# Kernel tuning notes

Hardware: AMD Instinct MI355X
Metric: run time of the kernel (lower is better)

The kernel has to match this reference:

```python
import jax, jax.numpy as jnp
import numpy as np

N = 50000          # nodes
E = 1000000        # edges
EMB = 64           # emb_dim
L = 3              # num_layer
B = 250            # graphs (200 nodes each)
XF, EF = 7, 5      # node / edge feature dims
BN_EPS = 1e-5


def setup_inputs() -> dict:
    key = jax.random.key(0)
    ks = jax.random.split(key, 16)
    x = jax.random.normal(ks[0], (N, XF), dtype=jnp.float32)
    edge_attr = jax.random.normal(ks[1], (E, EF), dtype=jnp.float32)
    edge_index = jax.random.randint(ks[2], (2, E), 0, N, dtype=jnp.int32)
    # 250 contiguous graphs of 200 nodes: last node index of each graph
    last_idx = jnp.arange(1, B + 1, dtype=jnp.int32) * (N // B) - 1
    s = 0.05
    xW = jax.random.normal(ks[3], (XF, EMB), dtype=jnp.float32) * s
    xb = jnp.zeros((EMB,), dtype=jnp.float32)
    eW = jax.random.normal(ks[4], (L, EF, EMB), dtype=jnp.float32) * s
    eb = jnp.zeros((L, EMB), dtype=jnp.float32)
    W1 = jax.random.normal(ks[5], (L, EMB, 2 * EMB), dtype=jnp.float32) * s
    b1 = jnp.zeros((L, 2 * EMB), dtype=jnp.float32)
    W2 = jax.random.normal(ks[6], (L, 2 * EMB, EMB), dtype=jnp.float32) * s
    b2 = jnp.zeros((L, EMB), dtype=jnp.float32)
    gamma = jnp.ones((L, EMB), dtype=jnp.float32)
    beta = jnp.zeros((L, EMB), dtype=jnp.float32)
    return {"x": x, "edge_attr": edge_attr, "edge_index": edge_index,
            "last_idx": last_idx, "xW": xW, "xb": xb, "eW": eW, "eb": eb,
            "W1": W1, "b1": b1, "W2": W2, "b2": b2,
            "gamma": gamma, "beta": beta}


def _gnn_forward(x, edge_attr, edge_index, last_idx, xW, xb, eW, eb, W1, b1, W2, b2, gamma, beta):
    n = x.shape[0]
    # self-loop edge attrs: first column = 8, rest 0
    self_attr = jnp.zeros((n, EF), dtype=edge_attr.dtype).at[:, 0].set(8.0)
    ea = jnp.concatenate([edge_attr, self_attr], axis=0)          # [E+N, EF]
    loop = jnp.arange(n, dtype=edge_index.dtype)
    src = jnp.concatenate([edge_index[0], loop])                  # x_j indices
    dst = jnp.concatenate([edge_index[1], loop])                  # aggregation targets

    h = x @ xW + xb                                               # [N, EMB]
    for l in range(L):
        e = ea @ eW[l] + eb[l]                                    # [E+N, EMB]
        msg = h[src] + e                                          # gather + combine
        agg = jax.ops.segment_sum(msg, dst, num_segments=n)       # scatter-add
        h2 = jax.nn.relu(agg @ W1[l] + b1[l]) @ W2[l] + b2[l]     # GIN MLP
        mean = jnp.mean(h2, axis=0)
        var = jnp.mean(jnp.square(h2 - mean), axis=0)             # biased, like torch BN
        hn = (h2 - mean) * jax.lax.rsqrt(var + BN_EPS) * gamma[l] + beta[l]
        h = jax.nn.elu(hn) if l < L - 1 else hn                   # drop_ratio = 0
    return h[last_idx]                                            # super-node reps [B, EMB]


def reference(x, edge_attr, edge_index, last_idx, xW, xb, eW, eb, W1, b1, W2, b2, gamma, beta):
    return _gnn_forward(x, edge_attr, edge_index, last_idx, xW, xb, eW, eb, W1, b1, W2, b2, gamma, beta)
```

## Files before the change

### kernel.cpp

```cpp
#include <hip/hip_runtime.h>

#define N_NODES 50000
#define N_EDGES 1000000
#define EMB     64
#define HID     128
#define NLAYER  3
#define NGRAPH  250
#define XFD     7
#define EFD     5
#define BN_EPS  1e-5f

#define BKT_SH 8
#define BKT_SZ 256
#define NBKT   ((N_NODES + BKT_SZ - 1) / BKT_SZ)
#define CHKE   4096
#define NCHK   ((N_EDGES + CHKE - 1) / CHKE)
#define CNTM   (NBKT * NCHK)
#define NB2    ((CNTM + 255) / 256)

__device__ __forceinline__ void atomAddF(float* p, float v) {
    __hip_atomic_fetch_add(p, v, __ATOMIC_RELAXED, __HIP_MEMORY_SCOPE_AGENT);
}

__device__ __forceinline__ unsigned short f2bf(float f) {
    unsigned int u = __float_as_uint(f);
    u += 0x7fffu + ((u >> 16) & 1u);
    return (unsigned short)(u >> 16);
}
__device__ __forceinline__ float bf2f(unsigned short s) {
    return __uint_as_float(((unsigned int)s) << 16);
}
__device__ __forceinline__ float4 bf4(ushort4 u) {
    return make_float4(bf2f(u.x), bf2f(u.y), bf2f(u.z), bf2f(u.w));
}

__global__ void k_input(const float* __restrict__ x, const float* __restrict__ xW,
                        const float* __restrict__ xb, unsigned short* __restrict__ h) {
    int gid = blockIdx.x * 256 + threadIdx.x;
    if (gid >= N_NODES * EMB) return;
    int n = gid >> 6, f = gid & 63;
    float acc = xb[f];
#pragma unroll
    for (int k = 0; k < XFD; ++k) acc = fmaf(x[n * XFD + k], xW[k * EMB + f], acc);
    h[gid] = f2bf(acc);
}

__global__ __launch_bounds__(256) void k_binA(const int* __restrict__ dst,
                                              int* __restrict__ cntmat) {
    __shared__ int hist[NBKT];
    int tid = threadIdx.x, c = blockIdx.x;
    for (int i = tid; i < NBKT; i += 256) hist[i] = 0;
    __syncthreads();
    int e0 = c * CHKE, e1 = min(e0 + CHKE, N_EDGES);
    for (int i = e0 + tid; i < e1; i += 256) atomicAdd(&hist[dst[i] >> BKT_SH], 1);
    __syncthreads();
    for (int b = tid; b < NBKT; b += 256) cntmat[b * NCHK + c] = hist[b];
}

__global__ __launch_bounds__(256) void k_gscanA(const int* __restrict__ in, int n,
                                                int* __restrict__ bsum) {
    int tid = threadIdx.x, lane = tid & 63, wid = tid >> 6;
    int i = blockIdx.x * 256 + tid;
    int v = (i < n) ? in[i] : 0;
#pragma unroll
    for (int off = 32; off; off >>= 1) v += __shfl_down(v, off);
    __shared__ int ws[4];
    if (lane == 0) ws[wid] = v;
    __syncthreads();
    if (tid == 0) bsum[blockIdx.x] = ws[0] + ws[1] + ws[2] + ws[3];
}

__global__ __launch_bounds__(256) void k_gscanB(const int* __restrict__ bsum, int nb,
                                                int* __restrict__ boff) {
    int tid = threadIdx.x, lane = tid & 63, wid = tid >> 6;
    int v = (tid < nb) ? bsum[tid] : 0;
    int x = v;
#pragma unroll
    for (int off = 1; off < 64; off <<= 1) {
        int y = __shfl_up(x, off);
        if (lane >= off) x += y;
    }
    __shared__ int wtot[4];
    if (lane == 63) wtot[wid] = x;
    __syncthreads();
    int woff = 0;
    for (int w = 0; w < wid; ++w) woff += wtot[w];
    if (tid < nb) boff[tid] = woff + x - v;
}

__global__ __launch_bounds__(256) void k_gscanC(const int* __restrict__ in, int n,
                                                const int* __restrict__ boff,
                                                int* __restrict__ out) {
    int tid = threadIdx.x, lane = tid & 63, wid = tid >> 6;
    int i = blockIdx.x * 256 + tid;
    int v = (i < n) ? in[i] : 0;
    int x = v;
#pragma unroll
    for (int off = 1; off < 64; off <<= 1) {
        int y = __shfl_up(x, off);
        if (lane >= off) x += y;
    }
    __shared__ int wtot[4];
    if (lane == 63) wtot[wid] = x;
    __syncthreads();
    int woff = boff[blockIdx.x];
    for (int w = 0; w < wid; ++w) woff += wtot[w];
    if (i < n) out[i] = woff + x - v;
}

__global__ __launch_bounds__(256) void k_binC(const int* __restrict__ src,
                                              const int* __restrict__ dst,
                                              const int* __restrict__ off2,
                                              int2* __restrict__ bufSD) {
    __shared__ int cur[NBKT];
    int tid = threadIdx.x, c = blockIdx.x;
    for (int b = tid; b < NBKT; b += 256) cur[b] = off2[b * NCHK + c];
    __syncthreads();
    int e0 = c * CHKE, e1 = min(e0 + CHKE, N_EDGES);
    for (int i = e0 + tid; i < e1; i += 256) {
        int d = dst[i];
        int b = d >> BKT_SH;
        int p = atomicAdd(&cur[b], 1);
        bufSD[p] = make_int2(src[i], ((d & (BKT_SZ - 1)) << 20) | i);
    }
}

__global__ __launch_bounds__(256) void k_binD(const int2* __restrict__ bufSD,
                                              const int* __restrict__ off2,
                                              int* __restrict__ csr,
                                              int* __restrict__ csrE,
                                              int* __restrict__ rowstart) {
    __shared__ int hist[BKT_SZ];
    __shared__ int cur[BKT_SZ];
    __shared__ int wtot[4];
    int tid = threadIdx.x, b = blockIdx.x;
    int bstart = off2[b * NCHK];
    int bend = (b + 1 < NBKT) ? off2[(b + 1) * NCHK] : N_EDGES;
    hist[tid] = 0;
    __syncthreads();
    for (int j = bstart + tid; j < bend; j += 256)
        atomicAdd(&hist[bufSD[j].y >> 20], 1);
    __syncthreads();
    int lane = tid & 63, wid = tid >> 6;
    int v = hist[tid], x = v;
#pragma unroll
    for (int off = 1; off < 64; off <<= 1) {
        int y = __shfl_up(x, off);
        if (lane >= off) x += y;
    }
    if (lane == 63) wtot[wid] = x;
    __syncthreads();
    int woff = 0;
    for (int w = 0; w < wid; ++w) woff += wtot[w];
    int ex = woff + x - v;
    cur[tid] = ex;
    int node = b * BKT_SZ + tid;
    if (node < N_NODES) rowstart[node] = bstart + ex;
    if (b == NBKT - 1 && tid == 0) rowstart[N_NODES] = N_EDGES;
    __syncthreads();
    for (int j = bstart + tid; j < bend; j += 256) {
        int2 t = bufSD[j];
        int local = t.y >> 20;
        int p = atomicAdd(&cur[local], 1);
        csr[bstart + p] = t.x;
        csrE[bstart + p] = t.y & 0xFFFFF;
    }
}

__global__ __launch_bounds__(256) void k_aggE(const int* __restrict__ rowstart,
                                              const int* __restrict__ csrE,
                                              const float* __restrict__ ea,
                                              float* __restrict__ aggE) {
    int wid = (blockIdx.x * 256 + threadIdx.x) >> 6;
    int lane = threadIdx.x & 63;
    if (wid >= N_NODES) return;
    int j0 = rowstart[wid], j1 = rowstart[wid + 1];
    float s0 = 0.f, s1 = 0.f, s2 = 0.f, s3 = 0.f, s4 = 0.f;
    for (int j = j0 + lane; j < j1; j += 64) {
        int e = csrE[j];
        const float* p = ea + (size_t)e * EFD;
        s0 += p[0]; s1 += p[1]; s2 += p[2]; s3 += p[3]; s4 += p[4];
    }
#pragma unroll
    for (int off = 32; off; off >>= 1) {
        s0 += __shfl_down(s0, off);
        s1 += __shfl_down(s1, off);
        s2 += __shfl_down(s2, off);
        s3 += __shfl_down(s3, off);
        s4 += __shfl_down(s4, off);
    }
    if (lane == 0) {
        float* o = aggE + (size_t)wid * EFD;
        o[0] = s0; o[1] = s1; o[2] = s2; o[3] = s3; o[4] = s4;
    }
}

__global__ __launch_bounds__(256) void k_agg(const unsigned short* __restrict__ h,
                                             float* __restrict__ agg,
                                             const int* __restrict__ rowstart,
                                             const int* __restrict__ csr,
                                             const float* __restrict__ aggE,
                                             const float* __restrict__ eWl,
                                             const float* __restrict__ ebl) {
    int wid = (blockIdx.x * 256 + threadIdx.x) >> 6;
    int lane = threadIdx.x & 63;
    if (wid >= N_NODES) return;
    int n = wid;
    int lg = lane >> 4, lq = lane & 15;
    const ushort4* hb = (const ushort4*)h;
    int j0 = rowstart[n], j1 = rowstart[n + 1];
    float4 acc = make_float4(0.f, 0.f, 0.f, 0.f);
    int j = j0;
    while (j < j1) {
        int take = j1 - j;
        if (take > 64) take = 64;
        int myid = (lane < take) ? csr[j + lane] : 0;
        int nt = (take + 3) >> 2;
        int t = 0;
        for (; t + 4 <= nt; t += 4) {
            int e0 = t * 4 + lg, e1 = e0 + 4, e2 = e0 + 8, e3 = e0 + 12;
            int s0 = __shfl(myid, e0), s1 = __shfl(myid, e1),
                s2 = __shfl(myid, e2), s3 = __shfl(myid, e3);
            ushort4 u0 = hb[(size_t)s0 * 16 + lq];
            ushort4 u1 = hb[(size_t)s1 * 16 + lq];
            ushort4 u2 = hb[(size_t)s2 * 16 + lq];
            ushort4 u3 = hb[(size_t)s3 * 16 + lq];
            float4 v0 = bf4(u0), v1 = bf4(u1), v2 = bf4(u2), v3 = bf4(u3);
            if (e0 < take) { acc.x += v0.x; acc.y += v0.y; acc.z += v0.z; acc.w += v0.w; }
            if (e1 < take) { acc.x += v1.x; acc.y += v1.y; acc.z += v1.z; acc.w += v1.w; }
            if (e2 < take) { acc.x += v2.x; acc.y += v2.y; acc.z += v2.z; acc.w += v2.w; }
            if (e3 < take) { acc.x += v3.x; acc.y += v3.y; acc.z += v3.z; acc.w += v3.w; }
        }
        for (; t < nt; ++t) {
            int e = t * 4 + lg;
            int s = __shfl(myid, e);
            float4 v = bf4(hb[(size_t)s * 16 + lq]);
            if (e < take) { acc.x += v.x; acc.y += v.y; acc.z += v.z; acc.w += v.w; }
        }
        j += take;
    }
    acc.x += __shfl_xor(acc.x, 16); acc.y += __shfl_xor(acc.y, 16);
    acc.z += __shfl_xor(acc.z, 16); acc.w += __shfl_xor(acc.w, 16);
    acc.x += __shfl_xor(acc.x, 32); acc.y += __shfl_xor(acc.y, 32);
    acc.z += __shfl_xor(acc.z, 32); acc.w += __shfl_xor(acc.w, 32);
    const float4* eW4 = (const float4*)eWl;
    float4 ew0 = eW4[lq], ew1 = eW4[16 + lq], ew2 = eW4[32 + lq],
           ew3 = eW4[48 + lq], ew4 = eW4[64 + lq];
    float4 eb4 = ((const float4*)ebl)[lq];
    float a0 = aggE[n * 5 + 0], a1 = aggE[n * 5 + 1], a2 = aggE[n * 5 + 2],
          a3 = aggE[n * 5 + 3], a4 = aggE[n * 5 + 4];
    float c0 = a0 + 8.f;
    float ce = (float)(j1 - j0) + 1.f;
    float4 bb = bf4(hb[(size_t)n * 16 + lq]);
    bb.x = fmaf(c0, ew0.x, bb.x); bb.y = fmaf(c0, ew0.y, bb.y);
    bb.z = fmaf(c0, ew0.z, bb.z); bb.w = fmaf(c0, ew0.w, bb.w);
    bb.x = fmaf(a1, ew1.x, bb.x); bb.y = fmaf(a1, ew1.y, bb.y);
    bb.z = fmaf(a1, ew1.z, bb.z); bb.w = fmaf(a1, ew1.w, bb.w);
    bb.x = fmaf(a2, ew2.x, bb.x); bb.y = fmaf(a2, ew2.y, bb.y);
    bb.z = fmaf(a2, ew2.z, bb.z); bb.w = fmaf(a2, ew2.w, bb.w);
    bb.x = fmaf(a3, ew3.x, bb.x); bb.y = fmaf(a3, ew3.y, bb.y);
    bb.z = fmaf(a3, ew3.z, bb.z); bb.w = fmaf(a3, ew3.w, bb.w);
    bb.x = fmaf(a4, ew4.x, bb.x); bb.y = fmaf(a4, ew4.y, bb.y);
    bb.z = fmaf(a4, ew4.z, bb.z); bb.w = fmaf(a4, ew4.w, bb.w);
    bb.x = fmaf(ce, eb4.x, bb.x); bb.y = fmaf(ce, eb4.y, bb.y);
    bb.z = fmaf(ce, eb4.z, bb.z); bb.w = fmaf(ce, eb4.w, bb.w);
    if (lg == 0) {
        ((float4*)agg)[(size_t)n * 16 + lq] =
            make_float4(acc.x + bb.x, acc.y + bb.y, acc.z + bb.z, acc.w + bb.w);
    }
}

__global__ __launch_bounds__(256) void k_mlp1(const float* __restrict__ agg,
                                              unsigned short* __restrict__ hidden,
                                              const float* __restrict__ W1l,
                                              const float* __restrict__ b1l) {
    __shared__ float w1s[64 * 128];
    __shared__ float as[32 * 68];
    __shared__ float b1s[128];
    int tid = threadIdx.x;
    int n0 = blockIdx.x * 32;
    const float4* wg = (const float4*)W1l;
    float4* wsh = (float4*)w1s;
#pragma unroll
    for (int i = 0; i < 8; ++i) wsh[tid + i * 256] = wg[tid + i * 256];
    if (tid < 128) b1s[tid] = b1l[tid];
    const float4* ag4 = (const float4*)agg;
#pragma unroll
    for (int i = 0; i < 2; ++i) {
        int idx = tid + i * 256;
        int m = idx >> 4, kq = idx & 15;
        int nn = n0 + m;
        float4 v = make_float4(0.f, 0.f, 0.f, 0.f);
        if (nn < N_NODES) v = ag4[nn * 16 + kq];
        *(float4*)&as[m * 68 + kq * 4] = v;
    }
    __syncthreads();
    int j0 = (tid & 31) * 4;
    int m0 = (tid >> 5) * 4;
    float acc[4][4] = {};
#pragma unroll 8
    for (int k = 0; k < 64; ++k) {
        float4 w = *(const float4*)&w1s[k * 128 + j0];
        float a0 = as[(m0 + 0) * 68 + k];
        float a1 = as[(m0 + 1) * 68 + k];
        float a2 = as[(m0 + 2) * 68 + k];
        float a3 = as[(m0 + 3) * 68 + k];
        acc[0][0] = fmaf(a0, w.x, acc[0][0]); acc[0][1] = fmaf(a0, w.y, acc[0][1]);
        acc[0][2] = fmaf(a0, w.z, acc[0][2]); acc[0][3] = fmaf(a0, w.w, acc[0][3]);
        acc[1][0] = fmaf(a1, w.x, acc[1][0]); acc[1][1] = fmaf(a1, w.y, acc[1][1]);
        acc[1][2] = fmaf(a1, w.z, acc[1][2]); acc[1][3] = fmaf(a1, w.w, acc[1][3]);
        acc[2][0] = fmaf(a2, w.x, acc[2][0]); acc[2][1] = fmaf(a2, w.y, acc[2][1]);
        acc[2][2] = fmaf(a2, w.z, acc[2][2]); acc[2][3] = fmaf(a2, w.w, acc[2][3]);
        acc[3][0] = fmaf(a3, w.x, acc[3][0]); acc[3][1] = fmaf(a3, w.y, acc[3][1]);
        acc[3][2] = fmaf(a3, w.z, acc[3][2]); acc[3][3] = fmaf(a3, w.w, acc[3][3]);
    }
    ushort4* hid4 = (ushort4*)hidden;
#pragma unroll
    for (int a = 0; a < 4; ++a) {
        int nn = n0 + m0 + a;
        if (nn < N_NODES) {
            ushort4 o;
            o.x = f2bf(fmaxf(acc[a][0] + b1s[j0 + 0], 0.f));
            o.y = f2bf(fmaxf(acc[a][1] + b1s[j0 + 1], 0.f));
            o.z = f2bf(fmaxf(acc[a][2] + b1s[j0 + 2], 0.f));
            o.w = f2bf(fmaxf(acc[a][3] + b1s[j0 + 3], 0.f));
            hid4[(size_t)nn * 32 + (j0 >> 2)] = o;
        }
    }
}

__global__ __launch_bounds__(256) void k_mlp2(const unsigned short* __restrict__ hidden,
                                              float* __restrict__ h2,
                                              const float* __restrict__ W2l,
                                              const float* __restrict__ b2l,
                                              float* __restrict__ stats) {
    __shared__ float w2s[128 * 64];
    __shared__ float hs[64 * 132];
    __shared__ float b2s[64];
    int tid = threadIdx.x;
    int n0 = blockIdx.x * 64;
    const float4* wg = (const float4*)W2l;
    float4* wsh = (float4*)w2s;
#pragma unroll
    for (int i = 0; i < 8; ++i) wsh[tid + i * 256] = wg[tid + i * 256];
    if (tid < 64) b2s[tid] = b2l[tid];
    const ushort4* hb4 = (const ushort4*)hidden;
#pragma unroll
    for (int i = 0; i < 8; ++i) {
        int idx = tid + i * 256;
        int m = idx >> 5, kq = idx & 31;
        int nn = n0 + m;
        float4 v = make_float4(0.f, 0.f, 0.f, 0.f);
        if (nn < N_NODES) v = bf4(hb4[(size_t)nn * 32 + kq]);
        *(float4*)&hs[m * 132 + kq * 4] = v;
    }
    __syncthreads();
    int f0 = (tid & 15) * 4;
    int m0 = (tid >> 4) * 4;
    float acc[4][4] = {};
#pragma unroll 8
    for (int k = 0; k < 128; ++k) {
        float4 w = *(const float4*)&w2s[k * 64 + f0];
        float a0 = hs[(m0 + 0) * 132 + k];
        float a1 = hs[(m0 + 1) * 132 + k];
        float a2 = hs[(m0 + 2) * 132 + k];
        float a3 = hs[(m0 + 3) * 132 + k];
        acc[0][0] = fmaf(a0, w.x, acc[0][0]); acc[0][1] = fmaf(a0, w.y, acc[0][1]);
        acc[0][2] = fmaf(a0, w.z, acc[0][2]); acc[0][3] = fmaf(a0, w.w, acc[0][3]);
        acc[1][0] = fmaf(a1, w.x, acc[1][0]); acc[1][1] = fmaf(a1, w.y, acc[1][1]);
        acc[1][2] = fmaf(a1, w.z, acc[1][2]); acc[1][3] = fmaf(a1, w.w, acc[1][3]);
        acc[2][0] = fmaf(a2, w.x, acc[2][0]); acc[2][1] = fmaf(a2, w.y, acc[2][1]);
        acc[2][2] = fmaf(a2, w.z, acc[2][2]); acc[2][3] = fmaf(a2, w.w, acc[2][3]);
        acc[3][0] = fmaf(a3, w.x, acc[3][0]); acc[3][1] = fmaf(a3, w.y, acc[3][1]);
        acc[3][2] = fmaf(a3, w.z, acc[3][2]); acc[3][3] = fmaf(a3, w.w, acc[3][3]);
    }
    float sf[4] = {0.f, 0.f, 0.f, 0.f}, qf[4] = {0.f, 0.f, 0.f, 0.f};
#pragma unroll
    for (int a = 0; a < 4; ++a) {
        int nn = n0 + m0 + a;
        if (nn < N_NODES) {
            float v0 = acc[a][0] + b2s[f0 + 0];
            float v1 = acc[a][1] + b2s[f0 + 1];
            float v2 = acc[a][2] + b2s[f0 + 2];
            float v3 = acc[a][3] + b2s[f0 + 3];
            *(float4*)&h2[nn * EMB + f0] = make_float4(v0, v1, v2, v3);
            sf[0] += v0; sf[1] += v1; sf[2] += v2; sf[3] += v3;
            qf[0] = fmaf(v0, v0, qf[0]); qf[1] = fmaf(v1, v1, qf[1]);
            qf[2] = fmaf(v2, v2, qf[2]); qf[3] = fmaf(v3, v3, qf[3]);
        }
    }
    __syncthreads();
    float* red = hs;
    int mg = tid >> 4;
#pragma unroll
    for (int j = 0; j < 4; ++j) {
        red[mg * 64 + f0 + j] = sf[j];
        red[1024 + mg * 64 + f0 + j] = qf[j];
    }
    __syncthreads();
    if (tid < 64) {
        float s = 0.f, q = 0.f;
#pragma unroll
        for (int m = 0; m < 16; ++m) {
            s += red[m * 64 + tid];
            q += red[1024 + m * 64 + tid];
        }
        atomAddF(&stats[tid], s);
        atomAddF(&stats[64 + tid], q);
    }
}

__global__ void k_bn(const float* __restrict__ h2, unsigned short* __restrict__ h,
                     const float* __restrict__ stats, const float* __restrict__ gam,
                     const float* __restrict__ bet) {
    int gid = blockIdx.x * 256 + threadIdx.x;
    if (gid >= N_NODES * EMB) return;
    int f = gid & 63;
    const float invN = 1.f / (float)N_NODES;
    float mean = stats[f] * invN;
    float var = stats[64 + f] * invN - mean * mean;
    float inv = rsqrtf(var + BN_EPS);
    float v = (h2[gid] - mean) * inv * gam[f] + bet[f];
    h[gid] = f2bf(v > 0.f ? v : expm1f(v));
}

__global__ void k_bnout(const float* __restrict__ h2, const int* __restrict__ last,
                        const float* __restrict__ stats, const float* __restrict__ gam,
                        const float* __restrict__ bet, float* __restrict__ out) {
    int gid = blockIdx.x * 256 + threadIdx.x;
    if (gid >= NGRAPH * EMB) return;
    int b = gid >> 6, f = gid & 63;
    const float invN = 1.f / (float)N_NODES;
    float mean = stats[f] * invN;
    float var = stats[64 + f] * invN - mean * mean;
    float inv = rsqrtf(var + BN_EPS);
    out[gid] = (h2[last[b] * EMB + f] - mean) * inv * gam[f] + bet[f];
}

extern "C" void kernel_launch(void* const* d_in, const int* in_sizes, int n_in,
                              void* d_out, int out_size, void* d_ws, size_t ws_size,
                              hipStream_t stream) {
    const float* x   = (const float*)d_in[0];
    const float* ea  = (const float*)d_in[1];
    const int*   eidx= (const int*)d_in[2];
    const int*   last= (const int*)d_in[3];
    const float* xW  = (const float*)d_in[4];
    const float* xb  = (const float*)d_in[5];
    const float* eW  = (const float*)d_in[6];
    const float* eb  = (const float*)d_in[7];
    const float* W1  = (const float*)d_in[8];
    const float* b1  = (const float*)d_in[9];
    const float* W2  = (const float*)d_in[10];
    const float* b2  = (const float*)d_in[11];
    const float* gam = (const float*)d_in[12];
    const float* bet = (const float*)d_in[13];
    float* out = (float*)d_out;

    const int* srcI = eidx;
    const int* dstI = eidx + N_EDGES;

    float* hslot  = (float*)d_ws;
    float* agg    = hslot + N_NODES * EMB;
    float* hidslot= agg + N_NODES * EMB;
    float* aggE   = hidslot + N_NODES * HID;
    float* stats  = aggE + NBKT * BKT_SZ * EFD;
    int* rowstart = (int*)(stats + NLAYER * 2 * EMB);
    int* csr      = rowstart + N_NODES + 1;
    int* cntmat   = csr + N_EDGES;
    int* off2     = cntmat + CNTM;
    int* bsum     = off2 + CNTM;
    int* boff     = bsum + NB2;
    unsigned short* h      = (unsigned short*)hslot;
    unsigned short* hidden = (unsigned short*)hidslot;
    int2* bufSD   = (int2*)agg;
    int*  csrE    = (int*)hidslot;

    hipMemsetAsync(stats, 0, NLAYER * 2 * EMB * sizeof(float), stream);

    k_input<<<(N_NODES * EMB + 255) / 256, 256, 0, stream>>>(x, xW, xb, h);
    k_binA<<<NCHK, 256, 0, stream>>>(dstI, cntmat);
    k_gscanA<<<NB2, 256, 0, stream>>>(cntmat, CNTM, bsum);
    k_gscanB<<<1, 256, 0, stream>>>(bsum, NB2, boff);
    k_gscanC<<<NB2, 256, 0, stream>>>(cntmat, CNTM, boff, off2);
    k_binC<<<NCHK, 256, 0, stream>>>(srcI, dstI, off2, bufSD);
    k_binD<<<NBKT, 256, 0, stream>>>(bufSD, off2, csr, csrE, rowstart);
    k_aggE<<<(N_NODES * 64 + 255) / 256, 256, 0, stream>>>(rowstart, csrE, ea, aggE);

    for (int l = 0; l < NLAYER; ++l) {
        k_agg<<<(N_NODES * 64 + 255) / 256, 256, 0, stream>>>(
            h, agg, rowstart, csr, aggE, eW + l * EFD * EMB, eb + l * EMB);
        k_mlp1<<<(N_NODES + 31) / 32, 256, 0, stream>>>(agg, hidden, W1 + l * EMB * HID,
                                                        b1 + l * HID);
        k_mlp2<<<(N_NODES + 63) / 64, 256, 0, stream>>>(hidden, agg, W2 + l * HID * EMB,
                                                        b2 + l * EMB, stats + l * 2 * EMB);
        if (l < NLAYER - 1) {
            k_bn<<<(N_NODES * EMB + 255) / 256, 256, 0, stream>>>(
                agg, h, stats + l * 2 * EMB, gam + l * EMB, bet + l * EMB);
        } else {
            k_bnout<<<(NGRAPH * EMB + 255) / 256, 256, 0, stream>>>(
                agg, last, stats + l * 2 * EMB, gam + l * EMB, bet + l * EMB, out);
        }
    }
}
```

Baseline: 409.3 us.

## Fuse GIN MLP layers into one kernel with bf16 LDS staging; batch agg nodes

Merges the two MLP kernels into a single k_mlp. The 128-wide hidden activation now stays in shared memory instead of making a round trip through global memory. Weights, inputs and the hidden tile are staged as bf16 in LDS, with transposed activation layouts, to keep shared-memory use down. k_agg now handles four nodes per wave so the edge-weight and bias loads are amortised, which reduces wave count and parallelism in the gather. The costs are lower precision for the MLP inputs and weights, higher LDS use per block, and k_mlp reading and writing the same agg buffer under __restrict__.

```diff
diff --git a/kernel.cpp b/kernel.cpp
--- a/kernel.cpp
+++ b/kernel.cpp
@@ -202,195 +202,186 @@
                                              const float* __restrict__ aggE,
                                              const float* __restrict__ eWl,
                                              const float* __restrict__ ebl) {
-    int wid = (blockIdx.x * 256 + threadIdx.x) >> 6;
+    int wave = (blockIdx.x * 256 + threadIdx.x) >> 6;
     int lane = threadIdx.x & 63;
-    if (wid >= N_NODES) return;
-    int n = wid;
+    int nbase = wave * 4;
+    if (nbase >= N_NODES) return;
     int lg = lane >> 4, lq = lane & 15;
     const ushort4* hb = (const ushort4*)h;
-    int j0 = rowstart[n], j1 = rowstart[n + 1];
-    float4 acc = make_float4(0.f, 0.f, 0.f, 0.f);
-    int j = j0;
-    while (j < j1) {
-        int take = j1 - j;
-        if (take > 64) take = 64;
-        int myid = (lane < take) ? csr[j + lane] : 0;
-        int nt = (take + 3) >> 2;
-        int t = 0;
-        for (; t + 4 <= nt; t += 4) {
-            int e0 = t * 4 + lg, e1 = e0 + 4, e2 = e0 + 8, e3 = e0 + 12;
-            int s0 = __shfl(myid, e0), s1 = __shfl(myid, e1),
-                s2 = __shfl(myid, e2), s3 = __shfl(myid, e3);
-            ushort4 u0 = hb[(size_t)s0 * 16 + lq];
-            ushort4 u1 = hb[(size_t)s1 * 16 + lq];
-            ushort4 u2 = hb[(size_t)s2 * 16 + lq];
-            ushort4 u3 = hb[(size_t)s3 * 16 + lq];
-            float4 v0 = bf4(u0), v1 = bf4(u1), v2 = bf4(u2), v3 = bf4(u3);
-            if (e0 < take) { acc.x += v0.x; acc.y += v0.y; acc.z += v0.z; acc.w += v0.w; }
-            if (e1 < take) { acc.x += v1.x; acc.y += v1.y; acc.z += v1.z; acc.w += v1.w; }
-            if (e2 < take) { acc.x += v2.x; acc.y += v2.y; acc.z += v2.z; acc.w += v2.w; }
-            if (e3 < take) { acc.x += v3.x; acc.y += v3.y; acc.z += v3.z; acc.w += v3.w; }
-        }
-        for (; t < nt; ++t) {
-            int e = t * 4 + lg;
-            int s = __shfl(myid, e);
-            float4 v = bf4(hb[(size_t)s * 16 + lq]);
-            if (e < take) { acc.x += v.x; acc.y += v.y; acc.z += v.z; acc.w += v.w; }
-        }
-        j += take;
-    }
-    acc.x += __shfl_xor(acc.x, 16); acc.y += __shfl_xor(acc.y, 16);
-    acc.z += __shfl_xor(acc.z, 16); acc.w += __shfl_xor(acc.w, 16);
-    acc.x += __shfl_xor(acc.x, 32); acc.y += __shfl_xor(acc.y, 32);
-    acc.z += __shfl_xor(acc.z, 32); acc.w += __shfl_xor(acc.w, 32);
     const float4* eW4 = (const float4*)eWl;
     float4 ew0 = eW4[lq], ew1 = eW4[16 + lq], ew2 = eW4[32 + lq],
            ew3 = eW4[48 + lq], ew4 = eW4[64 + lq];
     float4 eb4 = ((const float4*)ebl)[lq];
-    float a0 = aggE[n * 5 + 0], a1 = aggE[n * 5 + 1], a2 = aggE[n * 5 + 2],
-          a3 = aggE[n * 5 + 3], a4 = aggE[n * 5 + 4];
-    float c0 = a0 + 8.f;
-    float ce = (float)(j1 - j0) + 1.f;
-    float4 bb = bf4(hb[(size_t)n * 16 + lq]);
-    bb.x = fmaf(c0, ew0.x, bb.x); bb.y = fmaf(c0, ew0.y, bb.y);
-    bb.z = fmaf(c0, ew0.z, bb.z); bb.w = fmaf(c0, ew0.w, bb.w);
-    bb.x = fmaf(a1, ew1.x, bb.x); bb.y = fmaf(a1, ew1.y, bb.y);
-    bb.z = fmaf(a1, ew1.z, bb.z); bb.w = fmaf(a1, ew1.w, bb.w);
-    bb.x = fmaf(a2, ew2.x, bb.x); bb.y = fmaf(a2, ew2.y, bb.y);
-    bb.z = fmaf(a2, ew2.z, bb.z); bb.w = fmaf(a2, ew2.w, bb.w);
-    bb.x = fmaf(a3, ew3.x, bb.x); bb.y = fmaf(a3, ew3.y, bb.y);
-    bb.z = fmaf(a3, ew3.z, bb.z); bb.w = fmaf(a3, ew3.w, bb.w);
-    bb.x = fmaf(a4, ew4.x, bb.x); bb.y = fmaf(a4, ew4.y, bb.y);
-    bb.z = fmaf(a4, ew4.z, bb.z); bb.w = fmaf(a4, ew4.w, bb.w);
-    bb.x = fmaf(ce, eb4.x, bb.x); bb.y = fmaf(ce, eb4.y, bb.y);
-    bb.z = fmaf(ce, eb4.z, bb.z); bb.w = fmaf(ce, eb4.w, bb.w);
-    if (lg == 0) {
-        ((float4*)agg)[(size_t)n * 16 + lq] =
-            make_float4(acc.x + bb.x, acc.y + bb.y, acc.z + bb.z, acc.w + bb.w);
-    }
-}
-
-__global__ __launch_bounds__(256) void k_mlp1(const float* __restrict__ agg,
-                                              unsigned short* __restrict__ hidden,
-                                              const float* __restrict__ W1l,
-                                              const float* __restrict__ b1l) {
-    __shared__ float w1s[64 * 128];
-    __shared__ float as[32 * 68];
+    int nend = min(nbase + 4, N_NODES);
+    for (int n = nbase; n < nend; ++n) {
+        int j0 = rowstart[n], j1 = rowstart[n + 1];
+        float4 acc = make_float4(0.f, 0.f, 0.f, 0.f);
+        int j = j0;
+        while (j < j1) {
+            int take = j1 - j;
+            if (take > 64) take = 64;
+            int myid = (lane < take) ? csr[j + lane] : 0;
+            int nt = (take + 3) >> 2;
+            int t = 0;
+            for (; t + 4 <= nt; t += 4) {
+                int e0 = t * 4 + lg, e1 = e0 + 4, e2 = e0 + 8, e3 = e0 + 12;
+                int s0 = __shfl(myid, e0), s1 = __shfl(myid, e1),
+                    s2 = __shfl(myid, e2), s3 = __shfl(myid, e3);
+                float4 v0 = bf4(hb[(size_t)s0 * 16 + lq]);
+                float4 v1 = bf4(hb[(size_t)s1 * 16 + lq]);
+                float4 v2 = bf4(hb[(size_t)s2 * 16 + lq]);
+                float4 v3 = bf4(hb[(size_t)s3 * 16 + lq]);
+                if (e0 < take) { acc.x += v0.x; acc.y += v0.y; acc.z += v0.z; acc.w += v0.w; }
+                if (e1 < take) { acc.x += v1.x; acc.y += v1.y; acc.z += v1.z; acc.w += v1.w; }
+                if (e2 < take) { acc.x += v2.x; acc.y += v2.y; acc.z += v2.z; acc.w += v2.w; }
+                if (e3 < take) { acc.x += v3.x; acc.y += v3.y; acc.z += v3.z; acc.w += v3.w; }
+            }
+            for (; t < nt; ++t) {
+                int e = t * 4 + lg;
+                int s = __shfl(myid, e);
+                float4 v = bf4(hb[(size_t)s * 16 + lq]);
+                if (e < take) { acc.x += v.x; acc.y += v.y; acc.z += v.z; acc.w += v.w; }
+            }
+            j += take;
+        }
+        acc.x += __shfl_xor(acc.x, 16); acc.y += __shfl_xor(acc.y, 16);
+        acc.z += __shfl_xor(acc.z, 16); acc.w += __shfl_xor(acc.w, 16);
+        acc.x += __shfl_xor(acc.x, 32); acc.y += __shfl_xor(acc.y, 32);
+        acc.z += __shfl_xor(acc.z, 32); acc.w += __shfl_xor(acc.w, 32);
+        float a0 = aggE[n * 5 + 0], a1 = aggE[n * 5 + 1], a2 = aggE[n * 5 + 2],
+              a3 = aggE[n * 5 + 3], a4 = aggE[n * 5 + 4];
+        float c0 = a0 + 8.f;
+        float ce = (float)(j1 - j0) + 1.f;
+        float4 bb = bf4(hb[(size_t)n * 16 + lq]);
+        bb.x = fmaf(c0, ew0.x, bb.x); bb.y = fmaf(c0, ew0.y, bb.y);
+        bb.z = fmaf(c0, ew0.z, bb.z); bb.w = fmaf(c0, ew0.w, bb.w);
+        bb.x = fmaf(a1, ew1.x, bb.x); bb.y = fmaf(a1, ew1.y, bb.y);
+        bb.z = fmaf(a1, ew1.z, bb.z); bb.w = fmaf(a1, ew1.w, bb.w);
+        bb.x = fmaf(a2, ew2.x, bb.x); bb.y = fmaf(a2, ew2.y, bb.y);
+        bb.z = fmaf(a2, ew2.z, bb.z); bb.w = fmaf(a2, ew2.w, bb.w);
+        bb.x = fmaf(a3, ew3.x, bb.x); bb.y = fmaf(a3, ew3.y, bb.y);
+        bb.z = fmaf(a3, ew3.z, bb.z); bb.w = fmaf(a3, ew3.w, bb.w);
+        bb.x = fmaf(a4, ew4.x, bb.x); bb.y = fmaf(a4, ew4.y, bb.y);
+        bb.z = fmaf(a4, ew4.z, bb.z); bb.w = fmaf(a4, ew4.w, bb.w);
+        bb.x = fmaf(ce, eb4.x, bb.x); bb.y = fmaf(ce, eb4.y, bb.y);
+        bb.z = fmaf(ce, eb4.z, bb.z); bb.w = fmaf(ce, eb4.w, bb.w);
+        if (lg == 0) {
+            ((float4*)agg)[(size_t)n * 16 + lq] =
+                make_float4(acc.x + bb.x, acc.y + bb.y, acc.z + bb.z, acc.w + bb.w);
+        }
+    }
+}
+
+__global__ __launch_bounds__(256) void k_mlp(const float* __restrict__ agg,
+                                             float* __restrict__ h2,
+                                             const float* __restrict__ W1l,
+                                             const float* __restrict__ b1l,
+                                             const float* __restrict__ W2l,
+                                             const float* __restrict__ b2l,
+                                             float* __restrict__ stats) {
+    __shared__ unsigned short w1s[64 * 128];
+    __shared__ unsigned short w2s[128 * 64];
+    __shared__ unsigned short asT[64 * 68];
+    __shared__ unsigned short hidT[128 * 68];
     __shared__ float b1s[128];
+    __shared__ float b2s[64];
     int tid = threadIdx.x;
-    int n0 = blockIdx.x * 32;
-    const float4* wg = (const float4*)W1l;
-    float4* wsh = (float4*)w1s;
-#pragma unroll
-    for (int i = 0; i < 8; ++i) wsh[tid + i * 256] = wg[tid + i * 256];
+    int n0 = blockIdx.x * 64;
+    const float4* wg1 = (const float4*)W1l;
+    const float4* wg2 = (const float4*)W2l;
+    ushort4* w1v = (ushort4*)w1s;
+    ushort4* w2v = (ushort4*)w2s;
+#pragma unroll
+    for (int i = 0; i < 8; ++i) {
+        float4 v1 = wg1[tid + i * 256];
+        w1v[tid + i * 256] = make_ushort4(f2bf(v1.x), f2bf(v1.y), f2bf(v1.z), f2bf(v1.w));
+        float4 v2 = wg2[tid + i * 256];
+        w2v[tid + i * 256] = make_ushort4(f2bf(v2.x), f2bf(v2.y), f2bf(v2.z), f2bf(v2.w));
+    }
     if (tid < 128) b1s[tid] = b1l[tid];
+    if (tid < 64) b2s[tid] = b2l[tid];
     const float4* ag4 = (const float4*)agg;
 #pragma unroll
-    for (int i = 0; i < 2; ++i) {
+    for (int i = 0; i < 4; ++i) {
         int idx = tid + i * 256;
         int m = idx >> 4, kq = idx & 15;
         int nn = n0 + m;
         float4 v = make_float4(0.f, 0.f, 0.f, 0.f);
-        if (nn < N_NODES) v = ag4[nn * 16 + kq];
-        *(float4*)&as[m * 68 + kq * 4] = v;
-    }
-    __syncthreads();
-    int j0 = (tid & 31) * 4;
-    int m0 = (tid >> 5) * 4;
-    float acc[4][4] = {};
-#pragma unroll 8
-    for (int k = 0; k < 64; ++k) {
-        float4 w = *(const float4*)&w1s[k * 128 + j0];
-        float a0 = as[(m0 + 0) * 68 + k];
-        float a1 = as[(m0 + 1) * 68 + k];
-        float a2 = as[(m0 + 2) * 68 + k];
-        float a3 = as[(m0 + 3) * 68 + k];
-        acc[0][0] = fmaf(a0, w.x, acc[0][0]); acc[0][1] = fmaf(a0, w.y, acc[0][1]);
-        acc[0][2] = fmaf(a0, w.z, acc[0][2]); acc[0][3] = fmaf(a0, w.w, acc[0][3]);
-        acc[1][0] = fmaf(a1, w.x, acc[1][0]); acc[1][1] = fmaf(a1, w.y, acc[1][1]);
-        acc[1][2] = fmaf(a1, w.z, acc[1][2]); acc[1][3] = fmaf(a1, w.w, acc[1][3]);
-        acc[2][0] = fmaf(a2, w.x, acc[2][0]); acc[2][1] = fmaf(a2, w.y, acc[2][1]);
-        acc[2][2] = fmaf(a2, w.z, acc[2][2]); acc[2][3] = fmaf(a2, w.w, acc[2][3]);
-        acc[3][0] = fmaf(a3, w.x, acc[3][0]); acc[3][1] = fmaf(a3, w.y, acc[3][1]);
-        acc[3][2] = fmaf(a3, w.z, acc[3][2]); acc[3][3] = fmaf(a3, w.w, acc[3][3]);
-    }
-    ushort4* hid4 = (ushort4*)hidden;
-#pragma unroll
-    for (int a = 0; a < 4; ++a) {
-        int nn = n0 + m0 + a;
+        if (nn < N_NODES) v = ag4[(size_t)nn * 16 + kq];
+        asT[(kq * 4 + 0) * 68 + m] = f2bf(v.x);
+        asT[(kq * 4 + 1) * 68 + m] = f2bf(v.y);
+        asT[(kq * 4 + 2) * 68 + m] = f2bf(v.z);
+        asT[(kq * 4 + 3) * 68 + m] = f2bf(v.w);
+    }
+    __syncthreads();
+    {
+        int j0 = (tid & 31) * 4;
+        int m0 = (tid >> 5) * 8;
+        float acc1[8][4] = {};
+#pragma unroll 4
+        for (int k = 0; k < 64; ++k) {
+            float4 w = bf4(((const ushort4*)w1s)[k * 32 + (j0 >> 2)]);
+            float4 av0 = bf4(*(const ushort4*)&asT[k * 68 + m0]);
+            float4 av1 = bf4(*(const ushort4*)&asT[k * 68 + m0 + 4]);
+            float a[8] = {av0.x, av0.y, av0.z, av0.w, av1.x, av1.y, av1.z, av1.w};
+#pragma unroll
+            for (int i = 0; i < 8; ++i) {
+                acc1[i][0] = fmaf(a[i], w.x, acc1[i][0]);
+                acc1[i][1] = fmaf(a[i], w.y, acc1[i][1]);
+                acc1[i][2] = fmaf(a[i], w.z, acc1[i][2]);
+                acc1[i][3] = fmaf(a[i], w.w, acc1[i][3]);
+            }
+        }
+#pragma unroll
+        for (int c = 0; c < 4; ++c) {
+            float bv = b1s[j0 + c];
+            ushort4 o1, o2;
+            o1.x = f2bf(fmaxf(acc1[0][c] + bv, 0.f));
+            o1.y = f2bf(fmaxf(acc1[1][c] + bv, 0.f));
+            o1.z = f2bf(fmaxf(acc1[2][c] + bv, 0.f));
+            o1.w = f2bf(fmaxf(acc1[3][c] + bv, 0.f));
+            o2.x = f2bf(fmaxf(acc1[4][c] + bv, 0.f));
+            o2.y = f2bf(fmaxf(acc1[5][c] + bv, 0.f));
+            o2.z = f2bf(fmaxf(acc1[6][c] + bv, 0.f));
+            o2.w = f2bf(fmaxf(acc1[7][c] + bv, 0.f));
+            *(ushort4*)&hidT[(j0 + c) * 68 + m0] = o1;
+            *(ushort4*)&hidT[(j0 + c) * 68 + m0 + 4] = o2;
+        }
+    }
+    __syncthreads();
+    int f0 = (tid & 15) * 4;
+    int m0p = (tid >> 4) * 4;
+    float acc2[4][4] = {};
+#pragma unroll 4
+    for (int k = 0; k < 128; ++k) {
+        float4 w = bf4(((const ushort4*)w2s)[k * 16 + (f0 >> 2)]);
+        float4 a = bf4(*(const ushort4*)&hidT[k * 68 + m0p]);
+        acc2[0][0] = fmaf(a.x, w.x, acc2[0][0]); acc2[0][1] = fmaf(a.x, w.y, acc2[0][1]);
+        acc2[0][2] = fmaf(a.x, w.z, acc2[0][2]); acc2[0][3] = fmaf(a.x, w.w, acc2[0][3]);
+        acc2[1][0] = fmaf(a.y, w.x, acc2[1][0]); acc2[1][1] = fmaf(a.y, w.y, acc2[1][1]);
+        acc2[1][2] = fmaf(a.y, w.z, acc2[1][2]); acc2[1][3] = fmaf(a.y, w.w, acc2[1][3]);
+        acc2[2][0] = fmaf(a.z, w.x, acc2[2][0]); acc2[2][1] = fmaf(a.z, w.y, acc2[2][1]);
+        acc2[2][2] = fmaf(a.z, w.z, acc2[2][2]); acc2[2][3] = fmaf(a.z, w.w, acc2[2][3]);
+        acc2[3][0] = fmaf(a.w, w.x, acc2[3][0]); acc2[3][1] = fmaf(a.w, w.y, acc2[3][1]);
+        acc2[3][2] = fmaf(a.w, w.z, acc2[3][2]); acc2[3][3] = fmaf(a.w, w.w, acc2[3][3]);
+    }
+    float sf[4] = {0.f, 0.f, 0.f, 0.f}, qf[4] = {0.f, 0.f, 0.f, 0.f};
+#pragma unroll
+    for (int i = 0; i < 4; ++i) {
+        int nn = n0 + m0p + i;
         if (nn < N_NODES) {
-            ushort4 o;
-            o.x = f2bf(fmaxf(acc[a][0] + b1s[j0 + 0], 0.f));
-            o.y = f2bf(fmaxf(acc[a][1] + b1s[j0 + 1], 0.f));
-            o.z = f2bf(fmaxf(acc[a][2] + b1s[j0 + 2], 0.f));
-            o.w = f2bf(fmaxf(acc[a][3] + b1s[j0 + 3], 0.f));
-            hid4[(size_t)nn * 32 + (j0 >> 2)] = o;
-        }
-    }
-}
-
-__global__ __launch_bounds__(256) void k_mlp2(const unsigned short* __restrict__ hidden,
-                                              float* __restrict__ h2,
-                                              const float* __restrict__ W2l,
-                                              const float* __restrict__ b2l,
-                                              float* __restrict__ stats) {
-    __shared__ float w2s[128 * 64];
-    __shared__ float hs[64 * 132];
-    __shared__ float b2s[64];
-    int tid = threadIdx.x;
-    int n0 = blockIdx.x * 64;
-    const float4* wg = (const float4*)W2l;
-    float4* wsh = (float4*)w2s;
-#pragma unroll
-    for (int i = 0; i < 8; ++i) wsh[tid + i * 256] = wg[tid + i * 256];
-    if (tid < 64) b2s[tid] = b2l[tid];
-    const ushort4* hb4 = (const ushort4*)hidden;
-#pragma unroll
-    for (int i = 0; i < 8; ++i) {
-        int idx = tid + i * 256;
-        int m = idx >> 5, kq = idx & 31;
-        int nn = n0 + m;
-        float4 v = make_float4(0.f, 0.f, 0.f, 0.f);
-        if (nn < N_NODES) v = bf4(hb4[(size_t)nn * 32 + kq]);
-        *(float4*)&hs[m * 132 + kq * 4] = v;
-    }
-    __syncthreads();
-    int f0 = (tid & 15) * 4;
-    int m0 = (tid >> 4) * 4;
-    float acc[4][4] = {};
-#pragma unroll 8
-    for (int k = 0; k < 128; ++k) {
-        float4 w = *(const float4*)&w2s[k * 64 + f0];
-        float a0 = hs[(m0 + 0) * 132 + k];
-        float a1 = hs[(m0 + 1) * 132 + k];
-        float a2 = hs[(m0 + 2) * 132 + k];
-        float a3 = hs[(m0 + 3) * 132 + k];
-        acc[0][0] = fmaf(a0, w.x, acc[0][0]); acc[0][1] = fmaf(a0, w.y, acc[0][1]);
-        acc[0][2] = fmaf(a0, w.z, acc[0][2]); acc[0][3] = fmaf(a0, w.w, acc[0][3]);
-        acc[1][0] = fmaf(a1, w.x, acc[1][0]); acc[1][1] = fmaf(a1, w.y, acc[1][1]);
-        acc[1][2] = fmaf(a1, w.z, acc[1][2]); acc[1][3] = fmaf(a1, w.w, acc[1][3]);
-        acc[2][0] = fmaf(a2, w.x, acc[2][0]); acc[2][1] = fmaf(a2, w.y, acc[2][1]);
-        acc[2][2] = fmaf(a2, w.z, acc[2][2]); acc[2][3] = fmaf(a2, w.w, acc[2][3]);
-        acc[3][0] = fmaf(a3, w.x, acc[3][0]); acc[3][1] = fmaf(a3, w.y, acc[3][1]);
-        acc[3][2] = fmaf(a3, w.z, acc[3][2]); acc[3][3] = fmaf(a3, w.w, acc[3][3]);
-    }
-    float sf[4] = {0.f, 0.f, 0.f, 0.f}, qf[4] = {0.f, 0.f, 0.f, 0.f};
-#pragma unroll
-    for (int a = 0; a < 4; ++a) {
-        int nn = n0 + m0 + a;
-        if (nn < N_NODES) {
-            float v0 = acc[a][0] + b2s[f0 + 0];
-            float v1 = acc[a][1] + b2s[f0 + 1];
-            float v2 = acc[a][2] + b2s[f0 + 2];
-            float v3 = acc[a][3] + b2s[f0 + 3];
-            *(float4*)&h2[nn * EMB + f0] = make_float4(v0, v1, v2, v3);
+            float v0 = acc2[i][0] + b2s[f0 + 0];
+            float v1 = acc2[i][1] + b2s[f0 + 1];
+            float v2 = acc2[i][2] + b2s[f0 + 2];
+            float v3 = acc2[i][3] + b2s[f0 + 3];
+            *(float4*)&h2[(size_t)nn * EMB + f0] = make_float4(v0, v1, v2, v3);
             sf[0] += v0; sf[1] += v1; sf[2] += v2; sf[3] += v3;
             qf[0] = fmaf(v0, v0, qf[0]); qf[1] = fmaf(v1, v1, qf[1]);
             qf[2] = fmaf(v2, v2, qf[2]); qf[3] = fmaf(v3, v3, qf[3]);
         }
     }
     __syncthreads();
-    float* red = hs;
+    float* red = (float*)hidT;
     int mg = tid >> 4;
 #pragma unroll
     for (int j = 0; j < 4; ++j) {
@@ -470,8 +461,7 @@
     int* off2     = cntmat + CNTM;
     int* bsum     = off2 + CNTM;
     int* boff     = bsum + NB2;
-    unsigned short* h      = (unsigned short*)hslot;
-    unsigned short* hidden = (unsigned short*)hidslot;
+    unsigned short* h = (unsigned short*)hslot;
     int2* bufSD   = (int2*)agg;
     int*  csrE    = (int*)hidslot;
 
@@ -486,13 +476,14 @@
     k_binD<<<NBKT, 256, 0, stream>>>(bufSD, off2, csr, csrE, rowstart);
     k_aggE<<<(N_NODES * 64 + 255) / 256, 256, 0, stream>>>(rowstart, csrE, ea, aggE);
 
+    const int aggBlocks = ((N_NODES + 3) / 4 * 64 + 255) / 256;
+    const int mlpBlocks = (N_NODES + 63) / 64;
     for (int l = 0; l < NLAYER; ++l) {
-        k_agg<<<(N_NODES * 64 + 255) / 256, 256, 0, stream>>>(
+        k_agg<<<aggBlocks, 256, 0, stream>>>(
             h, agg, rowstart, csr, aggE, eW + l * EFD * EMB, eb + l * EMB);
-        k_mlp1<<<(N_NODES + 31) / 32, 256, 0, stream>>>(agg, hidden, W1 + l * EMB * HID,
-                                                        b1 + l * HID);
-        k_mlp2<<<(N_NODES + 63) / 64, 256, 0, stream>>>(hidden, agg, W2 + l * HID * EMB,
-                                                        b2 + l * EMB, stats + l * 2 * EMB);
+        k_mlp<<<mlpBlocks, 256, 0, stream>>>(agg, agg, W1 + l * EMB * HID, b1 + l * HID,
+                                             W2 + l * HID * EMB, b2 + l * EMB,
+                                             stats + l * 2 * EMB);
         if (l < NLAYER - 1) {
             k_bn<<<(N_NODES * EMB + 255) / 256, 256, 0, stream>>>(
                 agg, h, stats + l * 2 * EMB, gam + l * EMB, bet + l * EMB);
```

Result: faster. 400.4 us (-2.2%).
